# Kernel optimization log

Measured on AMD Instinct MI355X. Metric: run time of the kernel, lower is better.

## Reference

```python
import jax, jax.numpy as jnp
import numpy as np

IN_DIM, HID, OUT, N_EXTRA, NTASKS, BATCH = 1024, 2048, 10, 3, 10, 4096
LOGSTD_MEAN, LOGSTD_STD = -6.0, 0.1


def setup_inputs() -> dict:
    key = jax.random.key(0)
    ks = jax.random.split(key, 20)
    n = lambda k, s: jax.random.normal(k, s, dtype=jnp.float32)
    return {
        "x": n(ks[0], (BATCH, IN_DIM)),
        # shared layer 0 (in_dim -> hidden)
        "mu_w0": n(ks[1], (HID, IN_DIM)) * (1.0 / np.sqrt(IN_DIM)),
        "ls_w0": LOGSTD_MEAN + LOGSTD_STD * n(ks[2], (HID, IN_DIM)),
        "mu_b0": n(ks[3], (HID,)) * 0.01,
        "ls_b0": LOGSTD_MEAN + LOGSTD_STD * n(ks[4], (HID,)),
        # shared layers 1..3 (hidden -> hidden), stacked
        "mu_w": n(ks[5], (N_EXTRA, HID, HID)) * (1.0 / np.sqrt(HID)),
        "ls_w": LOGSTD_MEAN + LOGSTD_STD * n(ks[6], (N_EXTRA, HID, HID)),
        "mu_b": n(ks[7], (N_EXTRA, HID)) * 0.01,
        "ls_b": LOGSTD_MEAN + LOGSTD_STD * n(ks[8], (N_EXTRA, HID)),
        # per-task heads (hidden -> out), stacked over tasks
        "mu_hw": n(ks[9], (NTASKS, OUT, HID)) * (1.0 / np.sqrt(HID)),
        "ls_hw": LOGSTD_MEAN + LOGSTD_STD * n(ks[10], (NTASKS, OUT, HID)),
        "mu_hb": n(ks[11], (NTASKS, OUT)) * 0.01,
        "ls_hb": LOGSTD_MEAN + LOGSTD_STD * n(ks[12], (NTASKS, OUT)),
        # reparameterization noise (one sample per forward, as in torch module)
        "eps_w0": n(ks[13], (HID, IN_DIM)),
        "eps_b0": n(ks[14], (HID,)),
        "eps_w": n(ks[15], (N_EXTRA, HID, HID)),
        "eps_b": n(ks[16], (N_EXTRA, HID)),
        "eps_hw": n(ks[17], (NTASKS, OUT, HID)),
        "eps_hb": n(ks[18], (NTASKS, OUT)),
        "task": jax.random.randint(ks[19], (BATCH,), 0, NTASKS, dtype=jnp.int64),
    }


def reference(x, mu_w0, ls_w0, mu_b0, ls_b0, mu_w, ls_w, mu_b, ls_b,
              mu_hw, ls_hw, mu_hb, ls_hb,
              eps_w0, eps_b0, eps_w, eps_b, eps_hw, eps_hb, task):
    # BayesianLinear: w = mu + exp(log_sigma) * eps
    w0 = mu_w0 + jnp.exp(ls_w0) * eps_w0          # [HID, IN]
    b0 = mu_b0 + jnp.exp(ls_b0) * eps_b0          # [HID]
    h = jax.nn.relu(x @ w0.T + b0)                # [B, HID]
    for i in range(N_EXTRA):                      # fixed small layer loop
        wi = mu_w[i] + jnp.exp(ls_w[i]) * eps_w[i]
        bi = mu_b[i] + jnp.exp(ls_b[i]) * eps_b[i]
        h = jax.nn.relu(h @ wi.T + bi)
    # multihead: compute every head, zero out non-matching rows (dense masked)
    hw = mu_hw + jnp.exp(ls_hw) * eps_hw          # [T, OUT, HID]
    hb = mu_hb + jnp.exp(ls_hb) * eps_hb          # [T, OUT]
    out_all = jnp.einsum('bh,toh->bto', h, hw) + hb[None]   # [B, T, OUT]
    onehot = (task[:, None] == jnp.arange(NTASKS)[None, :]).astype(h.dtype)
    return jnp.einsum('bto,bt->bo', out_all, onehot)        # [B, OUT]
```

## Files before the change

### kernel.cpp

```cpp
#include <hip/hip_runtime.h>
#include <cstdint>

#define BATCH 4096
#define IN_DIM 1024
#define HID 2048
#define OUT_DIM 10
#define NTASKS 10

typedef __bf16 bf16x8 __attribute__((ext_vector_type(8)));
typedef float f32x4 __attribute__((ext_vector_type(4)));
typedef __attribute__((address_space(3))) uint8_t lds_u8;
typedef const __attribute__((address_space(1))) uint8_t glb_u8;

__device__ __forceinline__ unsigned short f2bf(float f) {
    uint32_t u = __builtin_bit_cast(uint32_t, f);
    u += 0x7fffu + ((u >> 16) & 1u);
    return (unsigned short)(u >> 16);
}
__device__ __forceinline__ float bf2f(unsigned short h) {
    uint32_t u = ((uint32_t)h) << 16;
    return __builtin_bit_cast(float, u);
}


__global__ __launch_bounds__(256) void bl_transform(
    const float4* __restrict__ mu, const float4* __restrict__ ls,
    const float4* __restrict__ eps, ushort4* __restrict__ out, int n4)
{
    int i = blockIdx.x * blockDim.x + threadIdx.x;
    const int stride = gridDim.x * blockDim.x;
    for (; i < n4; i += stride) {
        const float4 m = mu[i], l = ls[i], e = eps[i];
        ushort4 r;
        r.x = f2bf(m.x + __expf(l.x) * e.x);
        r.y = f2bf(m.y + __expf(l.y) * e.y);
        r.z = f2bf(m.z + __expf(l.z) * e.z);
        r.w = f2bf(m.w + __expf(l.w) * e.w);
        out[i] = r;
    }
}

__global__ __launch_bounds__(256) void bl_cvt(
    const float4* __restrict__ in, ushort4* __restrict__ out, int n4)
{
    int i = blockIdx.x * blockDim.x + threadIdx.x;
    const int stride = gridDim.x * blockDim.x;
    for (; i < n4; i += stride) {
        const float4 v = in[i];
        ushort4 r;
        r.x = f2bf(v.x); r.y = f2bf(v.y); r.z = f2bf(v.z); r.w = f2bf(v.w);
        out[i] = r;
    }
}

__global__ __launch_bounds__(256) void bl_small(
    const float* __restrict__ mu_b0, const float* __restrict__ ls_b0, const float* __restrict__ eps_b0,
    const float* __restrict__ mu_b,  const float* __restrict__ ls_b,  const float* __restrict__ eps_b,
    const float* __restrict__ mu_hw, const float* __restrict__ ls_hw, const float* __restrict__ eps_hw,
    const float* __restrict__ mu_hb, const float* __restrict__ ls_hb, const float* __restrict__ eps_hb,
    float* __restrict__ b_all, float* __restrict__ hw, float* __restrict__ hb)
{
    const int total = HID + 3*HID + NTASKS*OUT_DIM*HID + NTASKS*OUT_DIM;
    int i = blockIdx.x * blockDim.x + threadIdx.x;
    const int stride = gridDim.x * blockDim.x;
    for (; i < total; i += stride) {
        if (i < HID) {
            b_all[i] = mu_b0[i] + __expf(ls_b0[i]) * eps_b0[i];
        } else if (i < 4*HID) {
            const int j = i - HID;
            b_all[HID + j] = mu_b[j] + __expf(ls_b[j]) * eps_b[j];
        } else if (i < 4*HID + NTASKS*OUT_DIM*HID) {
            const int j = i - 4*HID;
            hw[j] = mu_hw[j] + __expf(ls_hw[j]) * eps_hw[j];
        } else {
            const int j = i - (4*HID + NTASKS*OUT_DIM*HID);
            hb[j] = mu_hb[j] + __expf(ls_hb[j]) * eps_hb[j];
        }
    }
}

#define BAR()        asm volatile("s_barrier" ::: "memory")
#define WAIT_LGKM0() do { asm volatile("s_waitcnt lgkmcnt(0)" ::: "memory"); __builtin_amdgcn_sched_barrier(0); } while (0)
#define RD_A(m, o)   (*(const bf16x8*)(ldsb + acur + (o) + (m)*2048))
#define RD_B(n, o)   (*(const bf16x8*)(ldsb + bcur + (o) + (n)*2048))
#define MFMA(d, va, vb) d = __builtin_amdgcn_mfma_f32_16x16x32_bf16(va, vb, d, 0, 0, 0)
#define STAGEI(i, kel, sl) \
    __builtin_amdgcn_global_load_lds((glb_u8*)(gsrc[i] + (kel)), \
        (lds_u8*)(ldsb + ldst[i] + (uint32_t)(sl) * smul[i]), 16, 0, 0)

__global__ __launch_bounds__(512, 2) void bl_gemm(
    const unsigned short* __restrict__ A,
    const unsigned short* __restrict__ B,
    const float* __restrict__ bias,
    unsigned short* __restrict__ C,
    int K)
{
    __shared__ unsigned short lds[49152];
    uint8_t* ldsb = (uint8_t*)lds;

    const int tid  = threadIdx.x;
    const int wave = tid >> 6;
    const int lane = tid & 63;
    const int swz = ((blockIdx.x & 7) << 5) | (blockIdx.x >> 3);
    const int bm = swz >> 4;
    const int bn = swz & 15;
    const int wr = wave >> 1;
    const int wc = wave & 1;

    const int lr8 = lane >> 3;
    const int ss  = (lane & 7) ^ lr8;
    const unsigned short* gsrc[6];
    uint32_t ldst[6], smul[6];
    #pragma unroll
    for (int i = 0; i < 6; ++i) {
        const int c = wave * 6 + i;
        if (c < 32) {
            gsrc[i] = A + (size_t)(bm * 256 + c * 8 + lr8) * K + ss * 8;
            ldst[i] = (uint32_t)c * 1024u;
            smul[i] = 32768u;
        } else {
            gsrc[i] = B + (size_t)(bn * 128 + (c - 32) * 8 + lr8) * K + ss * 8;
            ldst[i] = 65536u + (uint32_t)(c - 32) * 1024u;
            smul[i] = 16384u;
        }
    }

    const int rA = wr * 64 + (lane & 15);
    const int rB = wc * 64 + (lane & 15);
    const int ks = lane >> 4;
    const uint32_t aoff0 = (uint32_t)(rA * 128 + ((ks       ^ (rA & 7)) * 16));
    const uint32_t aoff1 = (uint32_t)(rA * 128 + (((4 | ks) ^ (rA & 7)) * 16));
    const uint32_t boff0 = (uint32_t)(rB * 128 + ((ks       ^ (rB & 7)) * 16));
    const uint32_t boff1 = (uint32_t)(rB * 128 + (((4 | ks) ^ (rB & 7)) * 16));

    f32x4 acc[4][4] = {};
    const int NT = K >> 6;

    STAGEI(0, 0, 0); STAGEI(1, 0, 0); STAGEI(2, 0, 0);
    STAGEI(3, 0, 0); STAGEI(4, 0, 0); STAGEI(5, 0, 0);
    __syncthreads();

    for (int t = 0; t < NT; ++t) {
        const int cur = t & 1, nxt = cur ^ 1;
        const uint32_t acur = (uint32_t)cur * 32768u;
        const uint32_t bcur = 65536u + (uint32_t)cur * 16384u;
        const bool pf = (t + 1 < NT);
        const int ktn = (t + 1) << 6;

        bf16x8 a0, a1, a2, a3, b0, b1, b2, b3;

        a0 = RD_A(0, aoff0); a1 = RD_A(1, aoff0);
        b0 = RD_B(0, boff0); b1 = RD_B(1, boff0); b2 = RD_B(2, boff0); b3 = RD_B(3, boff0);
        if (pf) { STAGEI(0, ktn, nxt); STAGEI(1, ktn, nxt); STAGEI(2, ktn, nxt); }
        BAR(); WAIT_LGKM0();
        __builtin_amdgcn_s_setprio(1);
        MFMA(acc[0][0], a0, b0); MFMA(acc[0][1], a0, b1); MFMA(acc[0][2], a0, b2); MFMA(acc[0][3], a0, b3);
        MFMA(acc[1][0], a1, b0); MFMA(acc[1][1], a1, b1); MFMA(acc[1][2], a1, b2); MFMA(acc[1][3], a1, b3);
        __builtin_amdgcn_s_setprio(0);
        BAR();

        a2 = RD_A(2, aoff0); a3 = RD_A(3, aoff0);
        BAR(); WAIT_LGKM0();
        __builtin_amdgcn_s_setprio(1);
        MFMA(acc[2][0], a2, b0); MFMA(acc[2][1], a2, b1); MFMA(acc[2][2], a2, b2); MFMA(acc[2][3], a2, b3);
        MFMA(acc[3][0], a3, b0); MFMA(acc[3][1], a3, b1); MFMA(acc[3][2], a3, b2); MFMA(acc[3][3], a3, b3);
        __builtin_amdgcn_s_setprio(0);
        BAR();

        a0 = RD_A(0, aoff1); a1 = RD_A(1, aoff1);
        b0 = RD_B(0, boff1); b1 = RD_B(1, boff1); b2 = RD_B(2, boff1); b3 = RD_B(3, boff1);
        if (pf) { STAGEI(3, ktn, nxt); STAGEI(4, ktn, nxt); STAGEI(5, ktn, nxt); }
        BAR(); WAIT_LGKM0();
        __builtin_amdgcn_s_setprio(1);
        MFMA(acc[0][0], a0, b0); MFMA(acc[0][1], a0, b1); MFMA(acc[0][2], a0, b2); MFMA(acc[0][3], a0, b3);
        MFMA(acc[1][0], a1, b0); MFMA(acc[1][1], a1, b1); MFMA(acc[1][2], a1, b2); MFMA(acc[1][3], a1, b3);
        __builtin_amdgcn_s_setprio(0);
        BAR();

        a2 = RD_A(2, aoff1); a3 = RD_A(3, aoff1);
        BAR(); WAIT_LGKM0();
        __builtin_amdgcn_s_setprio(1);
        MFMA(acc[2][0], a2, b0); MFMA(acc[2][1], a2, b1); MFMA(acc[2][2], a2, b2); MFMA(acc[2][3], a2, b3);
        MFMA(acc[3][0], a3, b0); MFMA(acc[3][1], a3, b1); MFMA(acc[3][2], a3, b2); MFMA(acc[3][3], a3, b3);
        __builtin_amdgcn_s_setprio(0);
        __syncthreads();
    }

    const int col0 = bn * 128 + wc * 64 + (lane & 15);
    const int row0 = bm * 256 + wr * 64 + ((lane >> 4) << 2);
    #pragma unroll
    for (int n = 0; n < 4; ++n) {
        const int col = col0 + n * 16;
        const float bv = bias[col];
        #pragma unroll
        for (int m = 0; m < 4; ++m) {
            #pragma unroll
            for (int j = 0; j < 4; ++j) {
                float v = acc[m][n][j] + bv;
                v = v > 0.0f ? v : 0.0f;
                C[(size_t)(row0 + m * 16 + j) * HID + col] = f2bf(v);
            }
        }
    }
}

__global__ __launch_bounds__(256) void bl_head(
    const unsigned short* __restrict__ h,
    const float* __restrict__ hw,
    const float* __restrict__ hb,
    const int* __restrict__ task,
    float* __restrict__ out)
{
    const int wave = threadIdx.x >> 6, lane = threadIdx.x & 63;
    const int b = blockIdx.x * 4 + wave;
    const int t = task[b];
    const float* w = hw + (size_t)t * OUT_DIM * HID;
    const unsigned short* hr = h + (size_t)b * HID;

    float acc[OUT_DIM];
    #pragma unroll
    for (int o = 0; o < OUT_DIM; ++o) acc[o] = 0.0f;

    for (int i = 0; i < HID / 64; ++i) {
        const int k = i * 64 + lane;
        const float hv = bf2f(hr[k]);
        #pragma unroll
        for (int o = 0; o < OUT_DIM; ++o)
            acc[o] += hv * w[(size_t)o * HID + k];
    }
    #pragma unroll
    for (int o = 0; o < OUT_DIM; ++o) {
        float v = acc[o];
        #pragma unroll
        for (int s = 32; s > 0; s >>= 1) v += __shfl_down(v, s, 64);
        if (lane == 0) out[(size_t)b * OUT_DIM + o] = v + hb[t * OUT_DIM + o];
    }
}


extern "C" void kernel_launch(void* const* d_in, const int* in_sizes, int n_in,
                              void* d_out, int out_size, void* d_ws, size_t ws_size,
                              hipStream_t stream)
{
    const float* x      = (const float*)d_in[0];
    const float* mu_w0  = (const float*)d_in[1];
    const float* ls_w0  = (const float*)d_in[2];
    const float* mu_b0  = (const float*)d_in[3];
    const float* ls_b0  = (const float*)d_in[4];
    const float* mu_w   = (const float*)d_in[5];
    const float* ls_w   = (const float*)d_in[6];
    const float* mu_b   = (const float*)d_in[7];
    const float* ls_b   = (const float*)d_in[8];
    const float* mu_hw  = (const float*)d_in[9];
    const float* ls_hw  = (const float*)d_in[10];
    const float* mu_hb  = (const float*)d_in[11];
    const float* ls_hb  = (const float*)d_in[12];
    const float* eps_w0 = (const float*)d_in[13];
    const float* eps_b0 = (const float*)d_in[14];
    const float* eps_w  = (const float*)d_in[15];
    const float* eps_b  = (const float*)d_in[16];
    const float* eps_hw = (const float*)d_in[17];
    const float* eps_hb = (const float*)d_in[18];
    const int*   task   = (const int*)d_in[19];

    uint8_t* ws = (uint8_t*)d_ws;
    constexpr size_t X_OFF  = 0;
    constexpr size_t W0_OFF = X_OFF  + (size_t)BATCH * IN_DIM * 2;
    constexpr size_t W_OFF  = W0_OFF + (size_t)HID * IN_DIM * 2;
    constexpr size_t H0_OFF = W_OFF  + (size_t)3 * HID * HID * 2;
    constexpr size_t H1_OFF = H0_OFF + (size_t)BATCH * HID * 2;
    constexpr size_t B_OFF  = H1_OFF + (size_t)BATCH * HID * 2;
    constexpr size_t HW_OFF = B_OFF  + (size_t)4 * HID * 4;
    constexpr size_t HB_OFF = HW_OFF + (size_t)NTASKS * OUT_DIM * HID * 4;

    unsigned short* xbf = (unsigned short*)(ws + X_OFF);
    unsigned short* w0b = (unsigned short*)(ws + W0_OFF);
    unsigned short* wb  = (unsigned short*)(ws + W_OFF);
    unsigned short* h0  = (unsigned short*)(ws + H0_OFF);
    unsigned short* h1  = (unsigned short*)(ws + H1_OFF);
    float* ball = (float*)(ws + B_OFF);
    float* hwf  = (float*)(ws + HW_OFF);
    float* hbf  = (float*)(ws + HB_OFF);

    bl_cvt<<<1024, 256, 0, stream>>>((const float4*)x, (ushort4*)xbf, BATCH * IN_DIM / 4);
    bl_transform<<<1024, 256, 0, stream>>>((const float4*)mu_w0, (const float4*)ls_w0,
                                           (const float4*)eps_w0, (ushort4*)w0b, HID * IN_DIM / 4);
    bl_transform<<<2048, 256, 0, stream>>>((const float4*)mu_w, (const float4*)ls_w,
                                           (const float4*)eps_w, (ushort4*)wb, 3 * HID * HID / 4);
    bl_small<<<512, 256, 0, stream>>>(mu_b0, ls_b0, eps_b0, mu_b, ls_b, eps_b,
                                      mu_hw, ls_hw, eps_hw, mu_hb, ls_hb, eps_hb,
                                      ball, hwf, hbf);

    bl_gemm<<<256, 512, 0, stream>>>(xbf, w0b, ball,             h0, IN_DIM);
    bl_gemm<<<256, 512, 0, stream>>>(h0, wb,                     ball + HID,   h1, HID);
    bl_gemm<<<256, 512, 0, stream>>>(h1, wb + (size_t)HID*HID,   ball + 2*HID, h0, HID);
    bl_gemm<<<256, 512, 0, stream>>>(h0, wb + (size_t)2*HID*HID, ball + 3*HID, h1, HID);

    bl_head<<<BATCH / 4, 256, 0, stream>>>(h1, hwf, hbf, task, (float*)d_out);
}
```

Measured before the change: 204.0 us.

## Unroll elementwise kernels, issue GEMM prefetch earlier, vectorize head loads

The conversion and transform kernels now each process four float4 elements per thread with exact grid sizing instead of a grid-stride loop, so more loads are in flight per thread. In the GEMM main loop, the second half of the next-tile staging loads now starts one phase earlier to overlap better with the MFMAs. The head kernel reads hidden activations as 8-wide bf16 vectors and weights as float4 pairs instead of scalar loads. The exact grid sizing assumes the element counts divide evenly, and the earlier prefetch keeps more loads outstanding during compute.

```diff
diff --git a/kernel.cpp b/kernel.cpp
--- a/kernel.cpp
+++ b/kernel.cpp
@@ -25,32 +25,41 @@
 
 __global__ __launch_bounds__(256) void bl_transform(
     const float4* __restrict__ mu, const float4* __restrict__ ls,
-    const float4* __restrict__ eps, ushort4* __restrict__ out, int n4)
-{
-    int i = blockIdx.x * blockDim.x + threadIdx.x;
-    const int stride = gridDim.x * blockDim.x;
-    for (; i < n4; i += stride) {
-        const float4 m = mu[i], l = ls[i], e = eps[i];
-        ushort4 r;
-        r.x = f2bf(m.x + __expf(l.x) * e.x);
-        r.y = f2bf(m.y + __expf(l.y) * e.y);
-        r.z = f2bf(m.z + __expf(l.z) * e.z);
-        r.w = f2bf(m.w + __expf(l.w) * e.w);
-        out[i] = r;
-    }
+    const float4* __restrict__ eps, ushort4* __restrict__ out)
+{
+    const int i0 = blockIdx.x * 1024 + threadIdx.x;
+    const float4 m0 = mu[i0], m1 = mu[i0 + 256], m2 = mu[i0 + 512], m3 = mu[i0 + 768];
+    const float4 l0 = ls[i0], l1 = ls[i0 + 256], l2 = ls[i0 + 512], l3 = ls[i0 + 768];
+    const float4 e0 = eps[i0], e1 = eps[i0 + 256], e2 = eps[i0 + 512], e3 = eps[i0 + 768];
+    ushort4 r0, r1, r2, r3;
+    r0.x = f2bf(m0.x + __expf(l0.x) * e0.x); r0.y = f2bf(m0.y + __expf(l0.y) * e0.y);
+    r0.z = f2bf(m0.z + __expf(l0.z) * e0.z); r0.w = f2bf(m0.w + __expf(l0.w) * e0.w);
+    r1.x = f2bf(m1.x + __expf(l1.x) * e1.x); r1.y = f2bf(m1.y + __expf(l1.y) * e1.y);
+    r1.z = f2bf(m1.z + __expf(l1.z) * e1.z); r1.w = f2bf(m1.w + __expf(l1.w) * e1.w);
+    r2.x = f2bf(m2.x + __expf(l2.x) * e2.x); r2.y = f2bf(m2.y + __expf(l2.y) * e2.y);
+    r2.z = f2bf(m2.z + __expf(l2.z) * e2.z); r2.w = f2bf(m2.w + __expf(l2.w) * e2.w);
+    r3.x = f2bf(m3.x + __expf(l3.x) * e3.x); r3.y = f2bf(m3.y + __expf(l3.y) * e3.y);
+    r3.z = f2bf(m3.z + __expf(l3.z) * e3.z); r3.w = f2bf(m3.w + __expf(l3.w) * e3.w);
+    out[i0]       = r0;
+    out[i0 + 256] = r1;
+    out[i0 + 512] = r2;
+    out[i0 + 768] = r3;
 }
 
 __global__ __launch_bounds__(256) void bl_cvt(
-    const float4* __restrict__ in, ushort4* __restrict__ out, int n4)
-{
-    int i = blockIdx.x * blockDim.x + threadIdx.x;
-    const int stride = gridDim.x * blockDim.x;
-    for (; i < n4; i += stride) {
-        const float4 v = in[i];
-        ushort4 r;
-        r.x = f2bf(v.x); r.y = f2bf(v.y); r.z = f2bf(v.z); r.w = f2bf(v.w);
-        out[i] = r;
-    }
+    const float4* __restrict__ in, ushort4* __restrict__ out)
+{
+    const int i0 = blockIdx.x * 1024 + threadIdx.x;
+    const float4 v0 = in[i0], v1 = in[i0 + 256], v2 = in[i0 + 512], v3 = in[i0 + 768];
+    ushort4 r0, r1, r2, r3;
+    r0.x = f2bf(v0.x); r0.y = f2bf(v0.y); r0.z = f2bf(v0.z); r0.w = f2bf(v0.w);
+    r1.x = f2bf(v1.x); r1.y = f2bf(v1.y); r1.z = f2bf(v1.z); r1.w = f2bf(v1.w);
+    r2.x = f2bf(v2.x); r2.y = f2bf(v2.y); r2.z = f2bf(v2.z); r2.w = f2bf(v2.w);
+    r3.x = f2bf(v3.x); r3.y = f2bf(v3.y); r3.z = f2bf(v3.z); r3.w = f2bf(v3.w);
+    out[i0]       = r0;
+    out[i0 + 256] = r1;
+    out[i0 + 512] = r2;
+    out[i0 + 768] = r3;
 }
 
 __global__ __launch_bounds__(256) void bl_small(
@@ -160,6 +169,7 @@
         BAR();
 
         a2 = RD_A(2, aoff0); a3 = RD_A(3, aoff0);
+        if (pf) { STAGEI(3, ktn, nxt); STAGEI(4, ktn, nxt); STAGEI(5, ktn, nxt); }
         BAR(); WAIT_LGKM0();
         __builtin_amdgcn_s_setprio(1);
         MFMA(acc[2][0], a2, b0); MFMA(acc[2][1], a2, b1); MFMA(acc[2][2], a2, b2); MFMA(acc[2][3], a2, b3);
@@ -169,7 +179,6 @@
 
         a0 = RD_A(0, aoff1); a1 = RD_A(1, aoff1);
         b0 = RD_B(0, boff1); b1 = RD_B(1, boff1); b2 = RD_B(2, boff1); b3 = RD_B(3, boff1);
-        if (pf) { STAGEI(3, ktn, nxt); STAGEI(4, ktn, nxt); STAGEI(5, ktn, nxt); }
         BAR(); WAIT_LGKM0();
         __builtin_amdgcn_s_setprio(1);
         MFMA(acc[0][0], a0, b0); MFMA(acc[0][1], a0, b1); MFMA(acc[0][2], a0, b2); MFMA(acc[0][3], a0, b3);
@@ -221,12 +230,20 @@
     #pragma unroll
     for (int o = 0; o < OUT_DIM; ++o) acc[o] = 0.0f;
 
-    for (int i = 0; i < HID / 64; ++i) {
-        const int k = i * 64 + lane;
-        const float hv = bf2f(hr[k]);
+    #pragma unroll
+    for (int i = 0; i < HID / 512; ++i) {
+        const int k0 = (i * 64 + lane) * 8;
+        const bf16x8 hv8 = *(const bf16x8*)(hr + k0);
+        float hf[8];
         #pragma unroll
-        for (int o = 0; o < OUT_DIM; ++o)
-            acc[o] += hv * w[(size_t)o * HID + k];
+        for (int j = 0; j < 8; ++j) hf[j] = (float)hv8[j];
+        #pragma unroll
+        for (int o = 0; o < OUT_DIM; ++o) {
+            const float4 w0 = *(const float4*)(w + (size_t)o * HID + k0);
+            const float4 w1 = *(const float4*)(w + (size_t)o * HID + k0 + 4);
+            acc[o] += hf[0]*w0.x + hf[1]*w0.y + hf[2]*w0.z + hf[3]*w0.w
+                    + hf[4]*w1.x + hf[5]*w1.y + hf[6]*w1.z + hf[7]*w1.w;
+        }
     }
     #pragma unroll
     for (int o = 0; o < OUT_DIM; ++o) {
@@ -282,11 +299,11 @@
     float* hwf  = (float*)(ws + HW_OFF);
     float* hbf  = (float*)(ws + HB_OFF);
 
-    bl_cvt<<<1024, 256, 0, stream>>>((const float4*)x, (ushort4*)xbf, BATCH * IN_DIM / 4);
-    bl_transform<<<1024, 256, 0, stream>>>((const float4*)mu_w0, (const float4*)ls_w0,
-                                           (const float4*)eps_w0, (ushort4*)w0b, HID * IN_DIM / 4);
-    bl_transform<<<2048, 256, 0, stream>>>((const float4*)mu_w, (const float4*)ls_w,
-                                           (const float4*)eps_w, (ushort4*)wb, 3 * HID * HID / 4);
+    bl_cvt<<<BATCH * IN_DIM / 4096, 256, 0, stream>>>((const float4*)x, (ushort4*)xbf);
+    bl_transform<<<HID * IN_DIM / 4096, 256, 0, stream>>>(
+        (const float4*)mu_w0, (const float4*)ls_w0, (const float4*)eps_w0, (ushort4*)w0b);
+    bl_transform<<<3 * HID * HID / 4096, 256, 0, stream>>>(
+        (const float4*)mu_w, (const float4*)ls_w, (const float4*)eps_w, (ushort4*)wb);
     bl_small<<<512, 256, 0, stream>>>(mu_b0, ls_b0, eps_b0, mu_b, ls_b, eps_b,
                                       mu_hw, ls_hw, eps_hw, mu_hb, ls_hb, eps_hb,
                                       ball, hwf, hbf);
```

Result: slower. 214.0 us (+4.9%).
